# Kernel optimization log

Measured on AMD Instinct MI355X. Metric: run time of the kernel, lower is better.

The kernel has to match this reference:

```python
import jax, jax.numpy as jnp
import numpy as np

D_MODEL = 1024
HEADS = 16
D_K = D_MODEL // HEADS


def setup_inputs() -> dict:
    key = jax.random.key(0)
    ks = jax.random.split(key, 11)
    B, S = 4, 2048
    scale = 1.0 / np.sqrt(D_MODEL)
    return {
        "q": jax.random.normal(ks[0], (B, S, D_MODEL), jnp.float32),
        "k": jax.random.normal(ks[1], (B, S, D_MODEL), jnp.float32),
        "v": jax.random.normal(ks[2], (B, S, D_MODEL), jnp.float32),
        "wq": jax.random.normal(ks[3], (D_MODEL, D_MODEL), jnp.float32) * scale,
        "bq": jax.random.normal(ks[4], (D_MODEL,), jnp.float32) * 0.01,
        "wk": jax.random.normal(ks[5], (D_MODEL, D_MODEL), jnp.float32) * scale,
        "bk": jax.random.normal(ks[6], (D_MODEL,), jnp.float32) * 0.01,
        "wv": jax.random.normal(ks[7], (D_MODEL, D_MODEL), jnp.float32) * scale,
        "bv": jax.random.normal(ks[8], (D_MODEL,), jnp.float32) * 0.01,
        "wo": jax.random.normal(ks[9], (D_MODEL, D_MODEL), jnp.float32) * scale,
        "bo": jax.random.normal(ks[10], (D_MODEL,), jnp.float32) * 0.01,
    }


def reference(q, k, v, wq, bq, wk, bk, wv, bv, wo, bo):
    B, S, _ = q.shape
    # nn.Linear: x @ W^T + b
    qp = q @ wq.T + bq
    kp = k @ wk.T + bk
    vp = v @ wv.T + bv
    # [B, S, D] -> [B, H, S, d_k]
    def split_heads(x):
        return x.reshape(B, S, HEADS, D_K).transpose(0, 2, 1, 3)
    qh, kh, vh = split_heads(qp), split_heads(kp), split_heads(vp)
    # scaled dot-product attention (dropout p=0 -> identity)
    scores = jnp.einsum("bhsd,bhtd->bhst", qh, kh) / jnp.sqrt(jnp.float32(D_K)).astype(qh.dtype)
    attn = jax.nn.softmax(scores, axis=-1)
    ctx = jnp.einsum("bhst,bhtd->bhsd", attn, vh)
    # merge heads and output projection
    ctx = ctx.transpose(0, 2, 1, 3).reshape(B, S, D_MODEL)
    return ctx @ wo.T + bo
```

## Files before the change

kernel.cpp:

```cpp
#include <hip/hip_runtime.h>


typedef __attribute__((ext_vector_type(8))) short bf16x8;
typedef __attribute__((ext_vector_type(4))) float f32x4;
typedef unsigned int u32;

#define DEVI __device__ __forceinline__

static constexpr int S_LEN = 2048;
static constexpr int NH = 16;
static constexpr int DK = 64;
static constexpr float Q_SCALE = 0.125f * 1.44269504088896340736f;

DEVI unsigned short f2b(float f) {
    unsigned int u = __builtin_bit_cast(unsigned int, f);
    u += 0x7fffu + ((u >> 16) & 1u);
    return (unsigned short)(u >> 16);
}

DEVI u32 pkbf16(float a, float b) {
#if __has_builtin(__builtin_amdgcn_cvt_pk_bf16_f32)
    auto r = __builtin_amdgcn_cvt_pk_bf16_f32(a, b);
    return __builtin_bit_cast(u32, r);
#else
    return (u32)f2b(a) | ((u32)f2b(b) << 16);
#endif
}

DEVI f32x4 mfma16(bf16x8 a, bf16x8 b, f32x4 c) {
    return __builtin_amdgcn_mfma_f32_16x16x32_bf16(a, b, c, 0, 0, 0);
}

#define GLL16(g, l)                                                        \
    __builtin_amdgcn_global_load_lds(                                      \
        (const __attribute__((address_space(1))) u32*)(g),                 \
        (__attribute__((address_space(3))) u32*)(l), 16, 0, 0)

__global__ __launch_bounds__(256) void cvt3(
    const float* __restrict__ q, const float* __restrict__ k,
    const float* __restrict__ v, unsigned short* __restrict__ dq,
    unsigned short* __restrict__ dk, unsigned short* __restrict__ dv) {
    const int z = blockIdx.y;
    const float* src = z == 0 ? q : z == 1 ? k : v;
    unsigned short* dst = z == 0 ? dq : z == 1 ? dk : dv;
    long i = ((long)blockIdx.x * 256 + threadIdx.x) * 8;
    float4 v0 = *(const float4*)(src + i);
    float4 v1 = *(const float4*)(src + i + 4);
    uint4 o;
    o.x = pkbf16(v0.x, v0.y);
    o.y = pkbf16(v0.z, v0.w);
    o.z = pkbf16(v1.x, v1.y);
    o.w = pkbf16(v1.z, v1.w);
    *(uint4*)(dst + i) = o;
}

__global__ __launch_bounds__(256) void cvt_w(
    const float* __restrict__ a, const float* __restrict__ b,
    const float* __restrict__ c, const float* __restrict__ d,
    unsigned short* __restrict__ o) {
    const float* src = blockIdx.y == 0 ? a : blockIdx.y == 1 ? b
                     : blockIdx.y == 2 ? c : d;
    unsigned short* dst = o + (long)blockIdx.y * 1048576;
    long i = ((long)blockIdx.x * 256 + threadIdx.x) * 8;
    float4 v0 = *(const float4*)(src + i);
    float4 v1 = *(const float4*)(src + i + 4);
    uint4 ov;
    ov.x = pkbf16(v0.x, v0.y);
    ov.y = pkbf16(v0.z, v0.w);
    ov.z = pkbf16(v1.x, v1.y);
    ov.w = pkbf16(v1.z, v1.w);
    *(uint4*)(dst + i) = ov;
}

__global__ __launch_bounds__(256) void gemm_qkv(
    const unsigned short* __restrict__ aq, const unsigned short* __restrict__ ak,
    const unsigned short* __restrict__ av, const unsigned short* __restrict__ wqkv,
    const float* __restrict__ bq, const float* __restrict__ bk,
    const float* __restrict__ bv, unsigned short* __restrict__ qh,
    unsigned short* __restrict__ kh, unsigned short* __restrict__ vht) {
    __shared__ __align__(16) unsigned short As[2][128 * 32];
    __shared__ __align__(16) unsigned short Bs[2][128 * 32];
    const int tid = threadIdx.x;
    const int w = tid >> 6, l = tid & 63, l16 = l & 15, quad = l >> 4;
    const int wm = (w >> 1) * 64, wn = (w & 1) * 64;
    const int m0 = blockIdx.y * 128, n0 = blockIdx.x * 128;
    const int z = blockIdx.z;
    const unsigned short* A = z == 0 ? aq : z == 1 ? ak : av;
    const unsigned short* W = wqkv + (long)z * 1048576;
    const float* bias = z == 0 ? bq : z == 1 ? bk : bv;

    f32x4 acc[4][4] = {};

    auto stage = [&](int kt, int buf) {
        #pragma unroll
        for (int h = 0; h < 2; ++h) {
            int sb = h * 256 + w * 64;
            int slot = sb + l;
            int row = slot >> 2, c = (slot & 3) ^ ((row >> 1) & 3);
            GLL16(A + (long)(m0 + row) * 1024 + kt + c * 8, &As[buf][sb * 8]);
            GLL16(W + (long)(n0 + row) * 1024 + kt + c * 8, &Bs[buf][sb * 8]);
        }
    };

    stage(0, 0);
    __syncthreads();

    for (int ki = 0; ki < 32; ++ki) {
        if (ki < 31) stage((ki + 1) * 32, (ki + 1) & 1);
        const unsigned short* as = As[ki & 1];
        const unsigned short* bs = Bs[ki & 1];
        bf16x8 a[4], b[4];
        #pragma unroll
        for (int i = 0; i < 4; ++i) {
            int r = wm + i * 16 + l16;
            a[i] = *(const bf16x8*)(as + (r * 4 + (quad ^ ((r >> 1) & 3))) * 8);
        }
        #pragma unroll
        for (int j = 0; j < 4; ++j) {
            int r = wn + j * 16 + l16;
            b[j] = *(const bf16x8*)(bs + (r * 4 + (quad ^ ((r >> 1) & 3))) * 8);
        }
        #pragma unroll
        for (int i = 0; i < 4; ++i)
            #pragma unroll
            for (int j = 0; j < 4; ++j)
                acc[i][j] = mfma16(a[i], b[j], acc[i][j]);
        __syncthreads();
    }

    if (z < 2) {
        unsigned short* out = z == 0 ? qh : kh;
        const float scale = z == 0 ? Q_SCALE : 1.0f;
        #pragma unroll
        for (int j = 0; j < 4; ++j) {
            int n = n0 + wn + j * 16 + l16;
            float bvl = bias[n];
            int hh = n >> 6, dd = n & 63;
            #pragma unroll
            for (int i = 0; i < 4; ++i)
                #pragma unroll
                for (int r = 0; r < 4; ++r) {
                    int m = m0 + wm + i * 16 + quad * 4 + r;
                    int bb = m >> 11, ss = m & 2047;
                    out[(((long)(bb * NH + hh) * S_LEN + ss) * DK) + dd] =
                        f2b((acc[i][j][r] + bvl) * scale);
                }
        }
    } else {
        unsigned short* out = vht;
        #pragma unroll
        for (int j = 0; j < 4; ++j) {
            int n = n0 + wn + j * 16 + l16;
            float bvl = bias[n];
            int hh = n >> 6, dd = n & 63;
            #pragma unroll
            for (int i = 0; i < 4; ++i) {
                int m = m0 + wm + i * 16 + quad * 4;
                int bb = m >> 11, ss = m & 2047;
                uint2 pk;
                pk.x = pkbf16(acc[i][j][0] + bvl, acc[i][j][1] + bvl);
                pk.y = pkbf16(acc[i][j][2] + bvl, acc[i][j][3] + bvl);
                *(uint2*)(out + ((long)(bb * NH + hh) * DK + dd) * S_LEN + ss) = pk;
            }
        }
    }
}

__global__ __launch_bounds__(256) void gemm_out(
    const unsigned short* __restrict__ A, const unsigned short* __restrict__ W,
    const float* __restrict__ bias, float* __restrict__ out) {
    __shared__ __align__(16) unsigned short As[2][128 * 32];
    __shared__ __align__(16) unsigned short Bs[2][128 * 32];
    const int tid = threadIdx.x;
    const int w = tid >> 6, l = tid & 63, l16 = l & 15, quad = l >> 4;
    const int wm = (w >> 1) * 64, wn = (w & 1) * 64;
    const int m0 = blockIdx.y * 128, n0 = blockIdx.x * 128;

    f32x4 acc[4][4] = {};

    auto stage = [&](int kt, int buf) {
        #pragma unroll
        for (int h = 0; h < 2; ++h) {
            int sb = h * 256 + w * 64;
            int slot = sb + l;
            int row = slot >> 2, c = (slot & 3) ^ ((row >> 1) & 3);
            GLL16(A + (long)(m0 + row) * 1024 + kt + c * 8, &As[buf][sb * 8]);
            GLL16(W + (long)(n0 + row) * 1024 + kt + c * 8, &Bs[buf][sb * 8]);
        }
    };

    stage(0, 0);
    __syncthreads();

    for (int ki = 0; ki < 32; ++ki) {
        if (ki < 31) stage((ki + 1) * 32, (ki + 1) & 1);
        const unsigned short* as = As[ki & 1];
        const unsigned short* bs = Bs[ki & 1];
        bf16x8 a[4], b[4];
        #pragma unroll
        for (int i = 0; i < 4; ++i) {
            int r = wm + i * 16 + l16;
            a[i] = *(const bf16x8*)(as + (r * 4 + (quad ^ ((r >> 1) & 3))) * 8);
        }
        #pragma unroll
        for (int j = 0; j < 4; ++j) {
            int r = wn + j * 16 + l16;
            b[j] = *(const bf16x8*)(bs + (r * 4 + (quad ^ ((r >> 1) & 3))) * 8);
        }
        #pragma unroll
        for (int i = 0; i < 4; ++i)
            #pragma unroll
            for (int j = 0; j < 4; ++j)
                acc[i][j] = mfma16(a[i], b[j], acc[i][j]);
        __syncthreads();
    }

    #pragma unroll
    for (int j = 0; j < 4; ++j) {
        int n = n0 + wn + j * 16 + l16;
        float bv = bias[n];
        #pragma unroll
        for (int i = 0; i < 4; ++i)
            #pragma unroll
            for (int r = 0; r < 4; ++r) {
                int m = m0 + wm + i * 16 + quad * 4 + r;
                out[(long)m * 1024 + n] = acc[i][j][r] + bv;
            }
    }
}

__global__ __launch_bounds__(256, 2) void attn(
    const unsigned short* __restrict__ qh, const unsigned short* __restrict__ kh,
    const unsigned short* __restrict__ vht, unsigned short* __restrict__ ctx) {
    __shared__ __align__(16) unsigned short Kb[2][8192];
    __shared__ __align__(16) unsigned short Vb[8192];
    __shared__ __align__(16) unsigned short P[128 * 44];

    const int bh = blockIdx.y, qt = blockIdx.x, tid = threadIdx.x;
    const int w = tid >> 6, l = tid & 63, l16 = l & 15, quad = l >> 4;

    const unsigned short* kh_b = kh + (long)bh * 2048 * 64;
    const unsigned short* vh_b = vht + (long)bh * 64 * 2048;

    const unsigned short* qsrc = qh + ((long)bh * 2048 + qt * 128) * 64;
    bf16x8 qf[2][2];
    #pragma unroll
    for (int dd = 0; dd < 2; ++dd)
        #pragma unroll
        for (int i = 0; i < 2; ++i)
            qf[dd][i] = *(const bf16x8*)(qsrc + (w * 32 + i * 16 + l16) * 64 +
                                         dd * 32 + quad * 8);

    #pragma unroll
    for (int rr = 0; rr < 4; ++rr) {
        int sb = (rr * 4 + w) * 64;
        int slot = sb + l;
        int row = slot >> 3, cc = (slot & 7) ^ (row & 7);
        GLL16(kh_b + (long)row * 64 + cc * 8, &Kb[0][sb * 8]);
    }
    __syncthreads();

    f32x4 o[4][2] = {};
    float lsum[2] = {0.f, 0.f};

    for (int kt = 0; kt < 16; ++kt) {
        if (kt < 15) {
            const unsigned short* kb_g = kh_b + (long)(kt + 1) * 128 * 64;
            #pragma unroll
            for (int rr = 0; rr < 4; ++rr) {
                int sb = (rr * 4 + w) * 64;
                int slot = sb + l;
                int row = slot >> 3, cc = (slot & 7) ^ (row & 7);
                GLL16(kb_g + (long)row * 64 + cc * 8, &Kb[(kt + 1) & 1][sb * 8]);
            }
        }
        {
            const unsigned short* vb_g = vh_b + kt * 128;
            #pragma unroll
            for (int rr = 0; rr < 4; ++rr) {
                int sb = (rr * 4 + w) * 64;
                int slot = sb + l;
                int d = slot >> 4, cc = (slot & 15) ^ (d & 15);
                GLL16(vb_g + (long)d * 2048 + cc * 8, &Vb[sb * 8]);
            }
        }

        const unsigned short* kb = Kb[kt & 1];
        f32x4 sa[2][8] = {};
        #pragma unroll
        for (int dd = 0; dd < 2; ++dd) {
            bf16x8 kf[8];
            #pragma unroll
            for (int ja = 0; ja < 8; ++ja) {
                int row = ja * 16 + l16;
                kf[ja] = *(const bf16x8*)(kb + (row * 8 + ((dd * 4 + quad) ^ (row & 7))) * 8);
            }
            #pragma unroll
            for (int i = 0; i < 2; ++i)
                #pragma unroll
                for (int ja = 0; ja < 8; ++ja)
                    sa[i][ja] = mfma16(kf[ja], qf[dd][i], sa[i][ja]);
        }

        #pragma unroll
        for (int i = 0; i < 2; ++i)
            #pragma unroll
            for (int ja = 0; ja < 8; ++ja)
                #pragma unroll
                for (int r = 0; r < 4; ++r) {
                    float p = exp2f(sa[i][ja][r]);
                    sa[i][ja][r] = p;
                    lsum[i] += p;
                }

        __syncthreads();

        #pragma unroll
        for (int qtr = 0; qtr < 4; ++qtr) {
            #pragma unroll
            for (int jh = 0; jh < 2; ++jh)
                #pragma unroll
                for (int i = 0; i < 2; ++i) {
                    int row = w * 32 + i * 16 + l16;
                    int ja = qtr * 2 + jh;
                    uint2 pk;
                    pk.x = pkbf16(sa[i][ja][0], sa[i][ja][1]);
                    pk.y = pkbf16(sa[i][ja][2], sa[i][ja][3]);
                    *(uint2*)(&P[row * 44 + jh * 16 + quad * 4]) = pk;
                }
            bf16x8 vf[4], pf[2];
            #pragma unroll
            for (int jd = 0; jd < 4; ++jd) {
                int d = jd * 16 + l16;
                vf[jd] = *(const bf16x8*)(Vb + (d * 16 + ((qtr * 4 + quad) ^ l16)) * 8);
            }
            #pragma unroll
            for (int i = 0; i < 2; ++i) {
                int row = w * 32 + i * 16 + l16;
                pf[i] = *(const bf16x8*)(&P[row * 44 + quad * 8]);
            }
            #pragma unroll
            for (int jd = 0; jd < 4; ++jd)
                #pragma unroll
                for (int i = 0; i < 2; ++i)
                    o[jd][i] = mfma16(vf[jd], pf[i], o[jd][i]);
        }
        __syncthreads();
    }

    #pragma unroll
    for (int i = 0; i < 2; ++i) {
        lsum[i] += __shfl_xor(lsum[i], 16);
        lsum[i] += __shfl_xor(lsum[i], 32);
    }

    const int b = bh >> 4, hh = bh & 15;
    #pragma unroll
    for (int i = 0; i < 2; ++i) {
        float inv = 1.0f / lsum[i];
        int s = qt * 128 + w * 32 + i * 16 + l16;
        #pragma unroll
        for (int jd = 0; jd < 4; ++jd) {
            uint2 pk;
            pk.x = pkbf16(o[jd][i][0] * inv, o[jd][i][1] * inv);
            pk.y = pkbf16(o[jd][i][2] * inv, o[jd][i][3] * inv);
            *(uint2*)(&ctx[((long)(b * 2048 + s) * 1024) + hh * 64 + jd * 16 + quad * 4]) = pk;
        }
    }
}

extern "C" void kernel_launch(void* const* d_in, const int* in_sizes, int n_in,
                              void* d_out, int out_size, void* d_ws, size_t ws_size,
                              hipStream_t stream) {
    const float* q  = (const float*)d_in[0];
    const float* k  = (const float*)d_in[1];
    const float* v  = (const float*)d_in[2];
    const float* wq = (const float*)d_in[3];
    const float* bq = (const float*)d_in[4];
    const float* wk = (const float*)d_in[5];
    const float* bk = (const float*)d_in[6];
    const float* wv = (const float*)d_in[7];
    const float* bv = (const float*)d_in[8];
    const float* wo = (const float*)d_in[9];
    const float* bo = (const float*)d_in[10];
    float* out = (float*)d_out;

    const size_t NE = 8u * 1024u * 1024u;
    unsigned short* ab_q = (unsigned short*)d_ws;
    unsigned short* qh   = ab_q + NE;
    unsigned short* kh   = qh + NE;
    unsigned short* vht  = kh + NE;
    unsigned short* wb   = vht + NE;
    unsigned short* wob  = wb + 3 * 1048576;
    unsigned short* ctx  = ab_q;
    unsigned short* ab_k = (unsigned short*)d_out;
    unsigned short* ab_v = ab_k + NE;

    dim3 blk(256);
    cvt_w<<<dim3(512, 4), blk, 0, stream>>>(wq, wk, wv, wo, wb);
    cvt3<<<dim3(4096, 3), blk, 0, stream>>>(q, k, v, ab_q, ab_k, ab_v);
    gemm_qkv<<<dim3(8, 64, 3), blk, 0, stream>>>(ab_q, ab_k, ab_v, wb,
                                                 bq, bk, bv, qh, kh, vht);
    attn<<<dim3(16, 64), blk, 0, stream>>>(qh, kh, vht, ctx);
    gemm_out<<<dim3(8, 64), blk, 0, stream>>>(ctx, wob, bo, out);
}
```

Before: 417.8 us.

## Reuse K buffer for P tile, raise attention occupancy, merge conversion kernels

The attention kernel drops its separate P shared-memory array. It writes the bf16 probabilities into the current K buffer, which is no longer needed once the scores are computed, using an XOR-swizzled layout. This cuts LDS use so launch bounds can ask for 3 blocks per CU. It also switches to the hardware exp2 intrinsic, keeps the row sums as vector accumulators, and splits the two QK halves so the first starts from a zero accumulator. The two fp32-to-bf16 conversion kernels are merged into one launch, and a faster fallback bf16 pack using perm is added. Possible costs are register pressure at higher occupancy and wasted idle blocks in the merged conversion grid.

```diff
diff --git a/kernel.cpp b/kernel.cpp
--- a/kernel.cpp
+++ b/kernel.cpp
@@ -23,7 +23,17 @@
     auto r = __builtin_amdgcn_cvt_pk_bf16_f32(a, b);
     return __builtin_bit_cast(u32, r);
 #else
-    return (u32)f2b(a) | ((u32)f2b(b) << 16);
+    u32 ua = __builtin_bit_cast(u32, a) + 0x8000u;
+    u32 ub = __builtin_bit_cast(u32, b) + 0x8000u;
+    return __builtin_amdgcn_perm(ub, ua, 0x07060302);
+#endif
+}
+
+DEVI float fexp2(float x) {
+#if __has_builtin(__builtin_amdgcn_exp2f)
+    return __builtin_amdgcn_exp2f(x);
+#else
+    return exp2f(x);
 #endif
 }
 
@@ -36,14 +46,29 @@
         (const __attribute__((address_space(1))) u32*)(g),                 \
         (__attribute__((address_space(3))) u32*)(l), 16, 0, 0)
 
-__global__ __launch_bounds__(256) void cvt3(
+__global__ __launch_bounds__(256) void cvt_all(
     const float* __restrict__ q, const float* __restrict__ k,
-    const float* __restrict__ v, unsigned short* __restrict__ dq,
-    unsigned short* __restrict__ dk, unsigned short* __restrict__ dv) {
+    const float* __restrict__ v, const float* __restrict__ wq,
+    const float* __restrict__ wk, const float* __restrict__ wv,
+    const float* __restrict__ wo, unsigned short* __restrict__ dq,
+    unsigned short* __restrict__ dk, unsigned short* __restrict__ dv,
+    unsigned short* __restrict__ dw) {
     const int z = blockIdx.y;
-    const float* src = z == 0 ? q : z == 1 ? k : v;
-    unsigned short* dst = z == 0 ? dq : z == 1 ? dk : dv;
-    long i = ((long)blockIdx.x * 256 + threadIdx.x) * 8;
+    const float* src;
+    unsigned short* dst;
+    long base;
+    if (z < 3) {
+        src = z == 0 ? q : z == 1 ? k : v;
+        dst = z == 0 ? dq : z == 1 ? dk : dv;
+        base = (long)blockIdx.x * 2048;
+    } else {
+        if (blockIdx.x >= 2048) return;
+        int wsel = blockIdx.x >> 9;
+        src = wsel == 0 ? wq : wsel == 1 ? wk : wsel == 2 ? wv : wo;
+        dst = dw + (long)wsel * 1048576;
+        base = (long)(blockIdx.x & 511) * 2048;
+    }
+    long i = base + threadIdx.x * 8;
     float4 v0 = *(const float4*)(src + i);
     float4 v1 = *(const float4*)(src + i + 4);
     uint4 o;
@@ -52,24 +77,6 @@
     o.z = pkbf16(v1.x, v1.y);
     o.w = pkbf16(v1.z, v1.w);
     *(uint4*)(dst + i) = o;
-}
-
-__global__ __launch_bounds__(256) void cvt_w(
-    const float* __restrict__ a, const float* __restrict__ b,
-    const float* __restrict__ c, const float* __restrict__ d,
-    unsigned short* __restrict__ o) {
-    const float* src = blockIdx.y == 0 ? a : blockIdx.y == 1 ? b
-                     : blockIdx.y == 2 ? c : d;
-    unsigned short* dst = o + (long)blockIdx.y * 1048576;
-    long i = ((long)blockIdx.x * 256 + threadIdx.x) * 8;
-    float4 v0 = *(const float4*)(src + i);
-    float4 v1 = *(const float4*)(src + i + 4);
-    uint4 ov;
-    ov.x = pkbf16(v0.x, v0.y);
-    ov.y = pkbf16(v0.z, v0.w);
-    ov.z = pkbf16(v1.x, v1.y);
-    ov.w = pkbf16(v1.z, v1.w);
-    *(uint4*)(dst + i) = ov;
 }
 
 __global__ __launch_bounds__(256) void gemm_qkv(
@@ -229,12 +236,11 @@
     }
 }
 
-__global__ __launch_bounds__(256, 2) void attn(
+__global__ __launch_bounds__(256, 3) void attn(
     const unsigned short* __restrict__ qh, const unsigned short* __restrict__ kh,
     const unsigned short* __restrict__ vht, unsigned short* __restrict__ ctx) {
     __shared__ __align__(16) unsigned short Kb[2][8192];
     __shared__ __align__(16) unsigned short Vb[8192];
-    __shared__ __align__(16) unsigned short P[128 * 44];
 
     const int bh = blockIdx.y, qt = blockIdx.x, tid = threadIdx.x;
     const int w = tid >> 6, l = tid & 63, l16 = l & 15, quad = l >> 4;
@@ -261,7 +267,7 @@
     __syncthreads();
 
     f32x4 o[4][2] = {};
-    float lsum[2] = {0.f, 0.f};
+    f32x4 ls4[2] = {};
 
     for (int kt = 0; kt < 16; ++kt) {
         if (kt < 15) {
@@ -285,73 +291,94 @@
             }
         }
 
-        const unsigned short* kb = Kb[kt & 1];
-        f32x4 sa[2][8] = {};
-        #pragma unroll
-        for (int dd = 0; dd < 2; ++dd) {
+        unsigned short* kb = (unsigned short*)Kb[kt & 1];
+        f32x4 sa[2][8];
+        {
+            const f32x4 z4 = {0.f, 0.f, 0.f, 0.f};
             bf16x8 kf[8];
             #pragma unroll
             for (int ja = 0; ja < 8; ++ja) {
                 int row = ja * 16 + l16;
-                kf[ja] = *(const bf16x8*)(kb + (row * 8 + ((dd * 4 + quad) ^ (row & 7))) * 8);
+                kf[ja] = *(const bf16x8*)(kb + (row * 8 + (quad ^ (row & 7))) * 8);
             }
             #pragma unroll
             for (int i = 0; i < 2; ++i)
                 #pragma unroll
                 for (int ja = 0; ja < 8; ++ja)
-                    sa[i][ja] = mfma16(kf[ja], qf[dd][i], sa[i][ja]);
+                    sa[i][ja] = mfma16(kf[ja], qf[0][i], z4);
+        }
+        {
+            bf16x8 kf[8];
+            #pragma unroll
+            for (int ja = 0; ja < 8; ++ja) {
+                int row = ja * 16 + l16;
+                kf[ja] = *(const bf16x8*)(kb + (row * 8 + ((4 + quad) ^ (row & 7))) * 8);
+            }
+            #pragma unroll
+            for (int i = 0; i < 2; ++i)
+                #pragma unroll
+                for (int ja = 0; ja < 8; ++ja)
+                    sa[i][ja] = mfma16(kf[ja], qf[1][i], sa[i][ja]);
         }
 
         #pragma unroll
         for (int i = 0; i < 2; ++i)
             #pragma unroll
-            for (int ja = 0; ja < 8; ++ja)
-                #pragma unroll
-                for (int r = 0; r < 4; ++r) {
-                    float p = exp2f(sa[i][ja][r]);
-                    sa[i][ja][r] = p;
-                    lsum[i] += p;
+            for (int ja = 0; ja < 8; ++ja) {
+                #pragma unroll
+                for (int r = 0; r < 4; ++r)
+                    sa[i][ja][r] = fexp2(sa[i][ja][r]);
+                ls4[i] += sa[i][ja];
+            }
+
+        __syncthreads();
+
+        #pragma unroll
+        for (int h = 0; h < 2; ++h) {
+            #pragma unroll
+            for (int ja = 0; ja < 4; ++ja)
+                #pragma unroll
+                for (int i = 0; i < 2; ++i) {
+                    int q = w * 32 + i * 16 + l16;
+                    const f32x4& s = sa[i][h * 4 + ja];
+                    int c = (ja * 2 + (quad >> 1)) ^ (l16 & 7);
+                    uint2 pk;
+                    pk.x = pkbf16(s[0], s[1]);
+                    pk.y = pkbf16(s[2], s[3]);
+                    *(uint2*)(kb + q * 64 + c * 8 + (quad & 1) * 4) = pk;
                 }
-
+            #pragma unroll
+            for (int kl = 0; kl < 2; ++kl) {
+                int ks = h * 2 + kl;
+                bf16x8 vf[4], pf[2];
+                #pragma unroll
+                for (int jd = 0; jd < 4; ++jd) {
+                    int d = jd * 16 + l16;
+                    vf[jd] = *(const bf16x8*)(Vb + (d * 16 + ((ks * 4 + quad) ^ l16)) * 8);
+                }
+                #pragma unroll
+                for (int i = 0; i < 2; ++i) {
+                    int q = w * 32 + i * 16 + l16;
+                    pf[i] = *(const bf16x8*)(kb + q * 64 +
+                                             (((kl * 4 + quad) ^ (l16 & 7)) * 8));
+                }
+                #pragma unroll
+                for (int jd = 0; jd < 4; ++jd)
+                    #pragma unroll
+                    for (int i = 0; i < 2; ++i)
+                        o[jd][i] = mfma16(vf[jd], pf[i], o[jd][i]);
+            }
+        }
         __syncthreads();
-
-        #pragma unroll
-        for (int qtr = 0; qtr < 4; ++qtr) {
-            #pragma unroll
-            for (int jh = 0; jh < 2; ++jh)
-                #pragma unroll
-                for (int i = 0; i < 2; ++i) {
-                    int row = w * 32 + i * 16 + l16;
-                    int ja = qtr * 2 + jh;
-                    uint2 pk;
-                    pk.x = pkbf16(sa[i][ja][0], sa[i][ja][1]);
-                    pk.y = pkbf16(sa[i][ja][2], sa[i][ja][3]);
-                    *(uint2*)(&P[row * 44 + jh * 16 + quad * 4]) = pk;
-                }
-            bf16x8 vf[4], pf[2];
-            #pragma unroll
-            for (int jd = 0; jd < 4; ++jd) {
-                int d = jd * 16 + l16;
-                vf[jd] = *(const bf16x8*)(Vb + (d * 16 + ((qtr * 4 + quad) ^ l16)) * 8);
-            }
-            #pragma unroll
-            for (int i = 0; i < 2; ++i) {
-                int row = w * 32 + i * 16 + l16;
-                pf[i] = *(const bf16x8*)(&P[row * 44 + quad * 8]);
-            }
-            #pragma unroll
-            for (int jd = 0; jd < 4; ++jd)
-                #pragma unroll
-                for (int i = 0; i < 2; ++i)
-                    o[jd][i] = mfma16(vf[jd], pf[i], o[jd][i]);
-        }
-        __syncthreads();
-    }
-
+    }
+
+    float lsum[2];
     #pragma unroll
     for (int i = 0; i < 2; ++i) {
-        lsum[i] += __shfl_xor(lsum[i], 16);
-        lsum[i] += __shfl_xor(lsum[i], 32);
+        float s = ls4[i][0] + ls4[i][1] + ls4[i][2] + ls4[i][3];
+        s += __shfl_xor(s, 16);
+        s += __shfl_xor(s, 32);
+        lsum[i] = s;
     }
 
     const int b = bh >> 4, hh = bh & 15;
@@ -397,8 +424,8 @@
     unsigned short* ab_v = ab_k + NE;
 
     dim3 blk(256);
-    cvt_w<<<dim3(512, 4), blk, 0, stream>>>(wq, wk, wv, wo, wb);
-    cvt3<<<dim3(4096, 3), blk, 0, stream>>>(q, k, v, ab_q, ab_k, ab_v);
+    cvt_all<<<dim3(4096, 4), blk, 0, stream>>>(q, k, v, wq, wk, wv, wo,
+                                               ab_q, ab_k, ab_v, wb);
     gemm_qkv<<<dim3(8, 64, 3), blk, 0, stream>>>(ab_q, ab_k, ab_v, wb,
                                                  bq, bk, bv, qh, kh, vht);
     attn<<<dim3(16, 64), blk, 0, stream>>>(qh, kh, vht, ctx);
```

Result: slower. 444.4 us (+6.4%).
